# Performance work log

Hardware: AMD Instinct MI355X
Metric: run time of the kernel (lower is better)

The kernel has to match this reference:

```python
import jax, jax.numpy as jnp
import numpy as np

B, T, H, W, C = 2, 8, 64, 64, 192
WIN = (4, 8, 8)
SHIFT = (2, 4, 4)
HEADS = 6
HID = 4 * C
N = WIN[0] * WIN[1] * WIN[2]  # 256 tokens per window
CPB_HID = 512


def window_partition(x, win):
    b, t, h, w, c = x.shape
    x = x.reshape(b, t // win[0], win[0], h // win[1], win[1], w // win[2], win[2], c)
    x = x.transpose(0, 1, 3, 5, 2, 4, 6, 7)
    return x.reshape(-1, win[0] * win[1] * win[2], c)


def window_reverse(wins, win, b, t, h, w):
    x = wins.reshape(b, t // win[0], h // win[1], w // win[2], win[0], win[1], win[2], -1)
    x = x.transpose(0, 1, 4, 2, 5, 3, 6, 7)
    return x.reshape(b, t, h, w, -1)


def _rel_coords_table():
    axes = [np.arange(-(WIN[i] - 1), WIN[i], dtype=np.float32) for i in range(3)]
    tbl = np.stack(np.meshgrid(*axes, indexing='ij'), axis=-1)  # (2wt-1,2wh-1,2ww-1,3)
    for i in range(3):
        tbl[..., i] /= WIN[i] - 1
    tbl *= 8.0
    tbl = np.sign(tbl) * np.log2(np.abs(tbl) + 1.0) / np.log2(8.0)
    return tbl.reshape(-1, 3)


def _rel_pos_index():
    coords = np.stack(np.meshgrid(np.arange(WIN[0]), np.arange(WIN[1]), np.arange(WIN[2]), indexing='ij'))
    cf = coords.reshape(3, -1)
    rel = (cf[:, :, None] - cf[:, None, :]).transpose(1, 2, 0)
    rel[..., 0] += WIN[0] - 1
    rel[..., 1] += WIN[1] - 1
    rel[..., 2] += WIN[2] - 1
    rel[..., 0] *= (2 * WIN[1] - 1) * (2 * WIN[2] - 1)
    rel[..., 1] *= 2 * WIN[2] - 1
    return rel.sum(-1)  # (N, N) int


def _attn_mask():
    img = np.zeros((1, T, H, W, 1), dtype=np.float32)
    cnt = 0
    for d in (slice(-WIN[0]), slice(-WIN[0], -SHIFT[0]), slice(-SHIFT[0], None)):
        for h in (slice(-WIN[1]), slice(-WIN[1], -SHIFT[1]), slice(-SHIFT[1], None)):
            for w in (slice(-WIN[2]), slice(-WIN[2], -SHIFT[2]), slice(-SHIFT[2], None)):
                img[:, d, h, w, :] = cnt
                cnt += 1
    mw = window_partition(img, WIN).squeeze(-1)  # (nW, N)
    am = mw[:, None, :] - mw[:, :, None]
    return np.where(am != 0, -100.0, 0.0).astype(np.float32)


REL_TABLE = jnp.asarray(_rel_coords_table())      # (M, 3)
RPI = jnp.asarray(_rel_pos_index().reshape(-1))   # (N*N,)
MASK = jnp.asarray(_attn_mask())                  # (nW, N, N)


def _ln(x, g, b):
    m = x.mean(-1, keepdims=True)
    v = x.var(-1, keepdims=True)
    return (x - m) / jnp.sqrt(v + 1e-5) * g + b


def setup_inputs() -> dict:
    key = jax.random.key(0)
    ks = jax.random.split(key, 16)
    s = lambda fan: 1.0 / np.sqrt(fan)
    return {
        'x': jax.random.normal(ks[0], (B, T, H, W, C), jnp.float32),
        'qkv_w': jax.random.normal(ks[1], (3 * C, C), jnp.float32) * s(C),
        'qkv_b': jnp.zeros((3 * C,), jnp.float32),
        'proj_w': jax.random.normal(ks[2], (C, C), jnp.float32) * s(C),
        'proj_b': jnp.zeros((C,), jnp.float32),
        'cpb_w1': jax.random.normal(ks[3], (CPB_HID, 3), jnp.float32) * s(3),
        'cpb_b1': jnp.zeros((CPB_HID,), jnp.float32),
        'cpb_w2': jax.random.normal(ks[4], (HEADS, CPB_HID), jnp.float32) * s(CPB_HID),
        'logit_scale': jnp.log(10.0 * jnp.ones((HEADS, 1, 1), jnp.float32)),
        'norm1_g': jnp.ones((C,), jnp.float32),
        'norm1_b': jnp.zeros((C,), jnp.float32),
        'norm2_g': jnp.ones((C,), jnp.float32),
        'norm2_b': jnp.zeros((C,), jnp.float32),
        'fc1_w': jax.random.normal(ks[5], (HID, C), jnp.float32) * s(C),
        'fc1_b': jnp.zeros((HID,), jnp.float32),
        'fc2_w': jax.random.normal(ks[6], (C, HID), jnp.float32) * s(HID),
        'fc2_b': jnp.zeros((C,), jnp.float32),
    }


def reference(x, qkv_w, qkv_b, proj_w, proj_b, cpb_w1, cpb_b1, cpb_w2,
              logit_scale, norm1_g, norm1_b, norm2_g, norm2_b,
              fc1_w, fc1_b, fc2_w, fc2_b):
    shortcut = x
    # cyclic shift
    xs = jnp.roll(x, shift=(-SHIFT[0], -SHIFT[1], -SHIFT[2]), axis=(1, 2, 3))
    xw = window_partition(xs, WIN)  # (B*nW, N, C)
    B_ = xw.shape[0]
    d = C // HEADS
    qkv = (xw @ qkv_w.T + qkv_b).reshape(B_, N, 3, HEADS, d).transpose(2, 0, 3, 1, 4)
    q, k, v = qkv[0], qkv[1], qkv[2]  # (B_, h, N, d)
    # cosine attention (F.normalize eps=1e-12)
    qn = q / jnp.maximum(jnp.linalg.norm(q, axis=-1, keepdims=True), 1e-12)
    kn = k / jnp.maximum(jnp.linalg.norm(k, axis=-1, keepdims=True), 1e-12)
    attn = jnp.einsum('bhnd,bhmd->bhnm', qn, kn)
    scale = jnp.exp(jnp.minimum(logit_scale, jnp.log(100.0)))  # clamp at log(1/0.01)
    attn = attn * scale
    # continuous relative position bias
    tbl = jax.nn.relu(REL_TABLE @ cpb_w1.T + cpb_b1) @ cpb_w2.T  # (M, heads)
    bias = tbl[RPI].reshape(N, N, HEADS).transpose(2, 0, 1)      # (h, N, N)
    attn = attn + 16.0 * jax.nn.sigmoid(bias)[None]
    # shift mask
    nW = MASK.shape[0]
    attn = attn.reshape(B_ // nW, nW, HEADS, N, N) + MASK[None, :, None]
    attn = jax.nn.softmax(attn.reshape(B_, HEADS, N, N), axis=-1)
    out = jnp.einsum('bhnm,bhmd->bhnd', attn, v)
    out = out.transpose(0, 2, 1, 3).reshape(B_, N, C)
    out = out @ proj_w.T + proj_b
    xr = window_reverse(out, WIN, B, T, H, W)
    xr = jnp.roll(xr, shift=SHIFT, axis=(1, 2, 3))
    # SwinV2 res-post-norm residual
    x = shortcut + _ln(xr, norm1_g, norm1_b)
    h1 = jax.nn.gelu(x @ fc1_w.T + fc1_b, approximate=False)
    x = x + _ln(h1 @ fc2_w.T + fc2_b, norm2_g, norm2_b)
    return x
```

## Files before the change

kernel.cpp:

```cpp
#include <hip/hip_runtime.h>
#include <math.h>


typedef short short8 __attribute__((ext_vector_type(8)));
typedef short short4v __attribute__((ext_vector_type(4)));
typedef float f32x4 __attribute__((ext_vector_type(4)));

__device__ __forceinline__ short f2bf(float f) {
    union { float f; unsigned u; } v; v.f = f;
    unsigned r = v.u + 0x7FFF + ((v.u >> 16) & 1);
    return (short)(r >> 16);
}

__device__ __forceinline__ float gelu_fast(float x) {
    float s = x * x;
    float t = fmaf(0.044715f, s, 1.0f);
    float y = -1.5957691216057308f * x * t;
    return x / (1.0f + __expf(y));
}

__global__ __launch_bounds__(64) void pack_w_k(const float* __restrict__ w,
                                               short* __restrict__ dst, int K) {
    int lane = threadIdx.x;
    int ktn = K >> 5;
    int nt = blockIdx.x / ktn, kt = blockIdx.x % ktn;
    int r = lane & 15, q = lane >> 4;
    const float* src = w + (size_t)(nt * 16 + r) * K + kt * 32 + q * 8;
    short8 v;
#pragma unroll
    for (int j = 0; j < 8; j++) v[j] = f2bf(src[j]);
    ((short8*)dst)[(size_t)blockIdx.x * 64 + lane] = v;
}

__global__ __launch_bounds__(64) void cpb_table_k(const float* __restrict__ w1,
                                                  const float* __restrict__ b1,
                                                  const float* __restrict__ w2,
                                                  float* __restrict__ tbl6) {
    int m = blockIdx.x;
    int lane = threadIdx.x;
    int it = m / 225;
    int ih = (m / 15) % 15;
    int iw = m % 15;
    float r0 = (float)(it - 3) * (8.0f / 3.0f);
    float r1 = (float)(ih - 7) * (8.0f / 7.0f);
    float r2 = (float)(iw - 7) * (8.0f / 7.0f);
    float c0 = (r0 < 0.f ? -1.f : 1.f) * log2f(fabsf(r0) + 1.0f) * (1.0f / 3.0f);
    float c1 = (r1 < 0.f ? -1.f : 1.f) * log2f(fabsf(r1) + 1.0f) * (1.0f / 3.0f);
    float c2 = (r2 < 0.f ? -1.f : 1.f) * log2f(fabsf(r2) + 1.0f) * (1.0f / 3.0f);
    float hv[8];
#pragma unroll
    for (int j = 0; j < 8; j++) {
        int t = lane * 8 + j;
        hv[j] = fmaxf(0.0f, c0 * w1[3 * t] + c1 * w1[3 * t + 1] + c2 * w1[3 * t + 2] + b1[t]);
    }
#pragma unroll
    for (int head = 0; head < 6; head++) {
        float s = 0.f;
#pragma unroll
        for (int j = 0; j < 8; j++) s += hv[j] * w2[head * 512 + lane * 8 + j];
        s += __shfl_xor(s, 1);
        s += __shfl_xor(s, 2);
        s += __shfl_xor(s, 4);
        s += __shfl_xor(s, 8);
        s += __shfl_xor(s, 16);
        s += __shfl_xor(s, 32);
        if (lane == 0) tbl6[m * 6 + head] = s;
    }
}

__global__ __launch_bounds__(256) void bias_k(const float* __restrict__ tbl6,
                                              float* __restrict__ biasT) {
    int idx = blockIdx.x * 256 + threadIdx.x;
    int h = idx >> 16;
    int rem = idx & 65535;
    int jj = rem >> 8, ii = rem & 255;
    int dt = (ii >> 6) - (jj >> 6) + 3;
    int dh = ((ii >> 3) & 7) - ((jj >> 3) & 7) + 7;
    int dw = (ii & 7) - (jj & 7) + 7;
    int rel = dt * 225 + dh * 15 + dw;
    float v = tbl6[rel * 6 + h];
    biasT[idx] = 16.0f / (1.0f + expf(-v));
}

#define ZSTR 388
__global__ __launch_bounds__(256) void qkv_mfma_k(const float* __restrict__ x,
                                                  const short* __restrict__ wqp,
                                                  const float* __restrict__ qkv_b,
                                                  short* __restrict__ qbf,
                                                  short* __restrict__ kbf,
                                                  short* __restrict__ vtb) {
    __shared__ float Z[32 * ZSTR];
    int tid = threadIdx.x, lane = tid & 63, w = tid >> 6;
    int r = lane & 15, q = lane >> 4;
    int b_ = blockIdx.x >> 3, n0 = (blockIdx.x & 7) << 5;
    int b = b_ >> 7, win = b_ & 127;
    int wt = win >> 6, wh = (win >> 3) & 7, ww = win & 7;

    short8 af[2][6];
#pragma unroll
    for (int m = 0; m < 2; m++) {
        int n = n0 + m * 16 + r;
        int t0 = ((wt * 4 + (n >> 6)) + 2) & 7;
        int h0 = ((wh * 8 + ((n >> 3) & 7)) + 4) & 63;
        int w0 = ((ww * 8 + (n & 7)) + 4) & 63;
        const float* src = x + ((size_t)((b * 8 + t0) * 64 + h0) * 64 + w0) * 192 + q * 8;
#pragma unroll
        for (int kt = 0; kt < 6; kt++) {
            float4 x0 = *(const float4*)(src + kt * 32);
            float4 x1 = *(const float4*)(src + kt * 32 + 4);
            short8 v;
            v[0] = f2bf(x0.x); v[1] = f2bf(x0.y); v[2] = f2bf(x0.z); v[3] = f2bf(x0.w);
            v[4] = f2bf(x1.x); v[5] = f2bf(x1.y); v[6] = f2bf(x1.z); v[7] = f2bf(x1.w);
            af[m][kt] = v;
        }
    }

    for (int ntl = 0; ntl < 9; ntl++) {
        int nt = w * 9 + ntl;
        float bias = qkv_b[nt * 16 + r];
        short8 bfr[6];
#pragma unroll
        for (int kt = 0; kt < 6; kt++)
            bfr[kt] = ((const short8*)wqp)[(size_t)(nt * 6 + kt) * 64 + lane];
        f32x4 a0 = {bias, bias, bias, bias};
        f32x4 a1 = {bias, bias, bias, bias};
#pragma unroll
        for (int kt = 0; kt < 6; kt++) {
            a0 = __builtin_amdgcn_mfma_f32_16x16x32_bf16(af[0][kt], bfr[kt], a0, 0, 0, 0);
            a1 = __builtin_amdgcn_mfma_f32_16x16x32_bf16(af[1][kt], bfr[kt], a1, 0, 0, 0);
        }
        int col = nt * 16 + r;
        if (nt < 24) {
#pragma unroll
            for (int reg = 0; reg < 4; reg++) {
                Z[(q * 4 + reg) * ZSTR + col] = a0[reg];
                Z[(16 + q * 4 + reg) * ZSTR + col] = a1[reg];
            }
        } else {
            int ch = col - 384;
            int hh = ch >> 5, dd = ch & 31;
            short* vb = vtb + ((size_t)(b_ * 6 + hh) * 32 + dd) * 256 + n0;
            short4v p0, p1;
#pragma unroll
            for (int reg = 0; reg < 4; reg++) { p0[reg] = f2bf(a0[reg]); p1[reg] = f2bf(a1[reg]); }
            *(short4v*)(vb + q * 4) = p0;
            *(short4v*)(vb + 16 + q * 4) = p1;
        }
    }
    __syncthreads();
    for (int rw = tid; rw < 384; rw += 256) {
        int token = rw / 12, rr = rw - token * 12;
        int isq = rr < 6 ? 1 : 0;
        int h = isq ? rr : rr - 6;
        const float* rp = &Z[token * ZSTR + rr * 32];
        float ss = 0.f;
#pragma unroll
        for (int d = 0; d < 32; d++) ss += rp[d] * rp[d];
        float inv = 1.0f / fmaxf(sqrtf(ss), 1e-12f);
        short* dst = (isq ? qbf : kbf) + ((size_t)(b_ * 6 + h) * 256 + n0 + token) * 32;
#pragma unroll
        for (int d8 = 0; d8 < 4; d8++) {
            short8 v;
#pragma unroll
            for (int j = 0; j < 8; j++) v[j] = f2bf(rp[d8 * 8 + j] * inv);
            *(short8*)(dst + d8 * 8) = v;
        }
    }
}

#define KSTR 40
#define VSTR 264
#define PSTR 40
__global__ __launch_bounds__(256) void attn_mfma_k(const short* __restrict__ qbf,
                                                   const short* __restrict__ kbf,
                                                   const short* __restrict__ vtb,
                                                   const float* __restrict__ biasT,
                                                   const float* __restrict__ logit_scale,
                                                   float* __restrict__ att) {
    __shared__ short Ks[256 * KSTR];
    __shared__ short Vs[32 * VSTR];
    __shared__ short Ps[4][16 * PSTR];
    int tid = threadIdx.x, lane = tid & 63, w = tid >> 6;
    int r = lane & 15, q = lane >> 4;
    int b_ = blockIdx.x / 6, h = blockIdx.x % 6;
    size_t base = (size_t)(b_ * 6 + h) * 8192;

    const short8* kg = (const short8*)(kbf + base);
    const short8* vg = (const short8*)(vtb + base);
    for (int i = tid; i < 1024; i += 256) {
        short8 kv = kg[i];
        *(short8*)&Ks[(i >> 2) * KSTR + (i & 3) * 8] = kv;
        short8 vv = vg[i];
        *(short8*)&Vs[(i >> 5) * VSTR + (i & 31) * 8] = vv;
    }

    short8 qf[4];
#pragma unroll
    for (int mt = 0; mt < 4; mt++)
        qf[mt] = *(const short8*)(qbf + base + (size_t)(w * 64 + mt * 16 + r) * 32 + q * 8);

    float scale = __expf(fminf(logit_scale[h], 4.6051702f));
    float M = scale + 16.0f;
    int win = b_ & 127;
    int wt4 = (win >> 6) * 4, wh8 = ((win >> 3) & 7) * 8, ww8 = (win & 7) * 8;
    auto region = [&](int n) {
        int ts = wt4 + (n >> 6), hs = wh8 + ((n >> 3) & 7), wsv = ww8 + (n & 7);
        int rt = ts < 4 ? 0 : (ts < 6 ? 1 : 2);
        int rh = hs < 56 ? 0 : (hs < 60 ? 1 : 2);
        int rw = wsv < 56 ? 0 : (wsv < 60 ? 1 : 2);
        return rt * 9 + rh * 3 + rw;
    };
    int rowreg[4][4];
#pragma unroll
    for (int mt = 0; mt < 4; mt++)
#pragma unroll
        for (int reg = 0; reg < 4; reg++)
            rowreg[mt][reg] = region(w * 64 + mt * 16 + q * 4 + reg);

    f32x4 O[4][2];
    float lp[4][4];
#pragma unroll
    for (int mt = 0; mt < 4; mt++) {
        O[mt][0] = (f32x4){0.f, 0.f, 0.f, 0.f};
        O[mt][1] = (f32x4){0.f, 0.f, 0.f, 0.f};
#pragma unroll
        for (int reg = 0; reg < 4; reg++) lp[mt][reg] = 0.f;
    }
    __syncthreads();

    const float* bh = biasT + ((size_t)h << 16);
    for (int s = 0; s < 8; s++) {
        short8 kf0 = *(const short8*)&Ks[(s * 32 + r) * KSTR + q * 8];
        short8 kf1 = *(const short8*)&Ks[(s * 32 + 16 + r) * KSTR + q * 8];
        short8 vf0 = *(const short8*)&Vs[r * VSTR + s * 32 + q * 8];
        short8 vf1 = *(const short8*)&Vs[(16 + r) * VSTR + s * 32 + q * 8];
        int cr0 = region(s * 32 + r);
        int cr1 = region(s * 32 + 16 + r);
#pragma unroll
        for (int mt = 0; mt < 4; mt++) {
            f32x4 s0 = {0.f, 0.f, 0.f, 0.f};
            f32x4 s1 = {0.f, 0.f, 0.f, 0.f};
            s0 = __builtin_amdgcn_mfma_f32_16x16x32_bf16(qf[mt], kf0, s0, 0, 0, 0);
            s1 = __builtin_amdgcn_mfma_f32_16x16x32_bf16(qf[mt], kf1, s1, 0, 0, 0);
            int qcol = w * 64 + mt * 16 + q * 4;
            float4 b0 = *(const float4*)(bh + (size_t)(s * 32 + r) * 256 + qcol);
            float4 b1 = *(const float4*)(bh + (size_t)(s * 32 + 16 + r) * 256 + qcol);
#pragma unroll
            for (int reg = 0; reg < 4; reg++) {
                float bb0 = (reg == 0 ? b0.x : reg == 1 ? b0.y : reg == 2 ? b0.z : b0.w);
                float bb1 = (reg == 0 ? b1.x : reg == 1 ? b1.y : reg == 2 ? b1.z : b1.w);
                float v0 = s0[reg] * scale + bb0 + (cr0 == rowreg[mt][reg] ? 0.f : -100.f) - M;
                float v1 = s1[reg] * scale + bb1 + (cr1 == rowreg[mt][reg] ? 0.f : -100.f) - M;
                float p0 = __expf(v0);
                float p1 = __expf(v1);
                lp[mt][reg] += p0 + p1;
                Ps[w][(q * 4 + reg) * PSTR + r] = f2bf(p0);
                Ps[w][(q * 4 + reg) * PSTR + 16 + r] = f2bf(p1);
            }
            short8 pa = *(const short8*)&Ps[w][r * PSTR + q * 8];
            O[mt][0] = __builtin_amdgcn_mfma_f32_16x16x32_bf16(pa, vf0, O[mt][0], 0, 0, 0);
            O[mt][1] = __builtin_amdgcn_mfma_f32_16x16x32_bf16(pa, vf1, O[mt][1], 0, 0, 0);
        }
    }

#pragma unroll
    for (int mt = 0; mt < 4; mt++)
#pragma unroll
        for (int reg = 0; reg < 4; reg++) {
            float v = lp[mt][reg];
            v += __shfl_xor(v, 1);
            v += __shfl_xor(v, 2);
            v += __shfl_xor(v, 4);
            v += __shfl_xor(v, 8);
            lp[mt][reg] = 1.0f / v;
        }
#pragma unroll
    for (int mt = 0; mt < 4; mt++)
#pragma unroll
        for (int nt = 0; nt < 2; nt++)
#pragma unroll
            for (int reg = 0; reg < 4; reg++) {
                int query = w * 64 + mt * 16 + q * 4 + reg;
                att[((size_t)b_ * 256 + query) * 192 + h * 32 + nt * 16 + r] =
                    O[mt][nt][reg] * lp[mt][reg];
            }
}

__global__ __launch_bounds__(256) void proj_mfma_k(const float* __restrict__ att,
                                                   const short* __restrict__ wpp,
                                                   const float* __restrict__ proj_b,
                                                   const float* __restrict__ x,
                                                   const float* __restrict__ g1,
                                                   const float* __restrict__ b1n,
                                                   float* __restrict__ out,
                                                   short* __restrict__ xmb) {
    __shared__ float Z[32 * 196];
    __shared__ float ps[32][8];
    __shared__ float pss[32][8];
    __shared__ float mean_s[32], inv_s[32];
    int tid = threadIdx.x, lane = tid & 63, w = tid >> 6;
    int r = lane & 15, q = lane >> 4;
    int b_ = blockIdx.x >> 3, n0 = (blockIdx.x & 7) << 5;

    short8 af[2][6];
#pragma unroll
    for (int m = 0; m < 2; m++) {
        const float* src = att + ((size_t)b_ * 256 + n0 + m * 16 + r) * 192 + q * 8;
#pragma unroll
        for (int kt = 0; kt < 6; kt++) {
            float4 x0 = *(const float4*)(src + kt * 32);
            float4 x1 = *(const float4*)(src + kt * 32 + 4);
            short8 v;
            v[0] = f2bf(x0.x); v[1] = f2bf(x0.y); v[2] = f2bf(x0.z); v[3] = f2bf(x0.w);
            v[4] = f2bf(x1.x); v[5] = f2bf(x1.y); v[6] = f2bf(x1.z); v[7] = f2bf(x1.w);
            af[m][kt] = v;
        }
    }
    for (int ntl = 0; ntl < 3; ntl++) {
        int nt = w * 3 + ntl;
        f32x4 binit = *(const f32x4*)(proj_b + nt * 16 + q * 4);
        short8 bfr[6];
#pragma unroll
        for (int kt = 0; kt < 6; kt++)
            bfr[kt] = ((const short8*)wpp)[(size_t)(nt * 6 + kt) * 64 + lane];
        f32x4 a0 = binit, a1 = binit;
#pragma unroll
        for (int kt = 0; kt < 6; kt++) {
            a0 = __builtin_amdgcn_mfma_f32_16x16x32_bf16(bfr[kt], af[0][kt], a0, 0, 0, 0);
            a1 = __builtin_amdgcn_mfma_f32_16x16x32_bf16(bfr[kt], af[1][kt], a1, 0, 0, 0);
        }
        *(f32x4*)&Z[(r) * 196 + nt * 16 + q * 4] = a0;
        *(f32x4*)&Z[(16 + r) * 196 + nt * 16 + q * 4] = a1;
    }
    __syncthreads();
    {
        int token = tid >> 3, part = tid & 7;
        float s = 0.f, ss = 0.f;
        const float* zr = &Z[token * 196 + part * 24];
#pragma unroll
        for (int c = 0; c < 24; c++) { float v = zr[c]; s += v; ss += v * v; }
        ps[token][part] = s; pss[token][part] = ss;
    }
    __syncthreads();
    if (tid < 32) {
        float s = 0.f, ss = 0.f;
#pragma unroll
        for (int p = 0; p < 8; p++) { s += ps[tid][p]; ss += pss[tid][p]; }
        float mean = s * (1.0f / 192.0f);
        float var = ss * (1.0f / 192.0f) - mean * mean;
        mean_s[tid] = mean;
        inv_s[tid] = 1.0f / sqrtf(var + 1e-5f);
    }
    __syncthreads();
    int b = b_ >> 7, win = b_ & 127;
    int wt = win >> 6, wh = (win >> 3) & 7, ww = win & 7;
    for (int idx = tid; idx < 6144; idx += 256) {
        int token = idx / 192;
        int ch = idx - token * 192;
        int n = n0 + token;
        int t0 = ((wt * 4 + (n >> 6)) + 2) & 7;
        int h0 = ((wh * 8 + ((n >> 3) & 7)) + 4) & 63;
        int w0 = ((ww * 8 + (n & 7)) + 4) & 63;
        size_t gb = ((size_t)((b * 8 + t0) * 64 + h0) * 64 + w0) * 192;
        float v = (Z[token * 196 + ch] - mean_s[token]) * inv_s[token] * g1[ch] + b1n[ch];
        float o = x[gb + ch] + v;
        out[gb + ch] = o;
        xmb[gb + ch] = f2bf(o);
    }
}

#define XSTR 200
#define H2STR 264
#define ZFSTR 196
__global__ __launch_bounds__(512, 4) void mlp_mfma_k(const short* __restrict__ xmb,
                                                     const short* __restrict__ w1p,
                                                     const short* __restrict__ w2p,
                                                     const float* __restrict__ fc1_b,
                                                     const float* __restrict__ fc2_b,
                                                     const float* __restrict__ g2,
                                                     const float* __restrict__ b2,
                                                     float* __restrict__ out) {
    __shared__ short Buf[64 * XSTR + 64 * H2STR];
    short* Xs = Buf;
    short* Hs = Buf + 64 * XSTR;
    float* Z = (float*)Buf;
    __shared__ float mean_s[64], inv_s[64];
    int tid = threadIdx.x;
    int lane = tid & 63, w = tid >> 6;
    int r = lane & 15, q = lane >> 4;
    size_t tok0 = (size_t)blockIdx.x * 64;

    for (int i = tid; i < 1536; i += 512) {
        int token = i / 24, ch8 = (i - token * 24) * 8;
        short8 v = *(const short8*)(xmb + (tok0 + token) * 192 + ch8);
        *(short8*)&Xs[token * XSTR + ch8] = v;
    }
    __syncthreads();

    int mg = w >> 2;
    int ng = w & 3;
    f32x4 acc2[6];
#pragma unroll
    for (int i = 0; i < 6; i++) acc2[i] = (f32x4){0.f, 0.f, 0.f, 0.f};

    for (int c = 0; c < 3; c++) {
        {
            int ntg0 = c * 16 + 2 * w;
            f32x4 a[2][4];
#pragma unroll
            for (int ntl = 0; ntl < 2; ntl++) {
                f32x4 binit = *(const f32x4*)(fc1_b + (ntg0 + ntl) * 16 + q * 4);
#pragma unroll
                for (int m = 0; m < 4; m++) a[ntl][m] = binit;
            }
#pragma unroll
            for (int kt = 0; kt < 6; kt++) {
                short8 w0 = ((const short8*)w1p)[(size_t)((ntg0) * 6 + kt) * 64 + lane];
                short8 w1f = ((const short8*)w1p)[(size_t)((ntg0 + 1) * 6 + kt) * 64 + lane];
                short8 xb[4];
#pragma unroll
                for (int m = 0; m < 4; m++)
                    xb[m] = *(const short8*)&Xs[(m * 16 + r) * XSTR + kt * 32 + q * 8];
#pragma unroll
                for (int m = 0; m < 4; m++) {
                    a[0][m] = __builtin_amdgcn_mfma_f32_16x16x32_bf16(w0, xb[m], a[0][m], 0, 0, 0);
                    a[1][m] = __builtin_amdgcn_mfma_f32_16x16x32_bf16(w1f, xb[m], a[1][m], 0, 0, 0);
                }
            }
#pragma unroll
            for (int ntl = 0; ntl < 2; ntl++) {
                int hcol = (2 * w + ntl) * 16 + q * 4;
#pragma unroll
                for (int m = 0; m < 4; m++) {
                    short4v p;
#pragma unroll
                    for (int reg = 0; reg < 4; reg++) p[reg] = f2bf(gelu_fast(a[ntl][m][reg]));
                    *(short4v*)&Hs[(m * 16 + r) * H2STR + hcol] = p;
                }
            }
        }
        __syncthreads();

#pragma unroll
        for (int kk = 0; kk < 8; kk++) {
            short8 hb0 = *(const short8*)&Hs[((mg * 2) * 16 + r) * H2STR + kk * 32 + q * 8];
            short8 hb1 = *(const short8*)&Hs[((mg * 2 + 1) * 16 + r) * H2STR + kk * 32 + q * 8];
            int kkg = c * 8 + kk;
#pragma unroll
            for (int n = 0; n < 3; n++) {
                int ntz = ng * 3 + n;
                short8 wf = ((const short8*)w2p)[(size_t)(ntz * 24 + kkg) * 64 + lane];
                acc2[n * 2 + 0] = __builtin_amdgcn_mfma_f32_16x16x32_bf16(wf, hb0, acc2[n * 2 + 0], 0, 0, 0);
                acc2[n * 2 + 1] = __builtin_amdgcn_mfma_f32_16x16x32_bf16(wf, hb1, acc2[n * 2 + 1], 0, 0, 0);
            }
        }
        __syncthreads();
    }

#pragma unroll
    for (int n = 0; n < 3; n++) {
        int ntz = ng * 3 + n;
        f32x4 b4 = *(const f32x4*)(fc2_b + ntz * 16 + q * 4);
#pragma unroll
        for (int mh = 0; mh < 2; mh++) {
            int token = (mg * 2 + mh) * 16 + r;
            f32x4 zv = acc2[n * 2 + mh] + b4;
            *(f32x4*)&Z[token * ZFSTR + ntz * 16 + q * 4] = zv;
        }
    }
    __syncthreads();

    {
        int token = w * 8 + (lane >> 3), part = lane & 7;
        float s = 0.f, ss = 0.f;
        const float* zr = &Z[token * ZFSTR + part * 24];
#pragma unroll
        for (int ccc = 0; ccc < 24; ccc++) { float v = zr[ccc]; s += v; ss += v * v; }
        s += __shfl_xor(s, 1); ss += __shfl_xor(ss, 1);
        s += __shfl_xor(s, 2); ss += __shfl_xor(ss, 2);
        s += __shfl_xor(s, 4); ss += __shfl_xor(ss, 4);
        if (part == 0) {
            float mean = s * (1.0f / 192.0f);
            float var = ss * (1.0f / 192.0f) - mean * mean;
            mean_s[token] = mean;
            inv_s[token] = 1.0f / sqrtf(var + 1e-5f);
        }
    }
    __syncthreads();
    for (int rep = 0; rep < 24; rep++) {
        int idx = rep * 512 + tid;
        int token = idx / 192;
        int ch = idx - token * 192;
        float v = (Z[token * ZFSTR + ch] - mean_s[token]) * inv_s[token] * g2[ch] + b2[ch];
        size_t gi = (tok0 + token) * 192 + ch;
        out[gi] = out[gi] + v;
    }
}

extern "C" void kernel_launch(void* const* d_in, const int* in_sizes, int n_in,
                              void* d_out, int out_size, void* d_ws, size_t ws_size,
                              hipStream_t stream) {
    const float* x           = (const float*)d_in[0];
    const float* qkv_w       = (const float*)d_in[1];
    const float* qkv_b       = (const float*)d_in[2];
    const float* proj_w      = (const float*)d_in[3];
    const float* proj_b      = (const float*)d_in[4];
    const float* cpb_w1      = (const float*)d_in[5];
    const float* cpb_b1      = (const float*)d_in[6];
    const float* cpb_w2      = (const float*)d_in[7];
    const float* logit_scale = (const float*)d_in[8];
    const float* norm1_g     = (const float*)d_in[9];
    const float* norm1_b     = (const float*)d_in[10];
    const float* norm2_g     = (const float*)d_in[11];
    const float* norm2_b     = (const float*)d_in[12];
    const float* fc1_w       = (const float*)d_in[13];
    const float* fc1_b       = (const float*)d_in[14];
    const float* fc2_w       = (const float*)d_in[15];
    const float* fc2_b       = (const float*)d_in[16];
    float* out = (float*)d_out;

    float* ws = (float*)d_ws;
    const size_t QKVE = (size_t)256 * 6 * 256 * 32;
    float* att    = ws;
    float* biasT  = att + QKVE;
    float* tbl6   = biasT + (size_t)6 * 256 * 256;
    short* w1pack = (short*)(tbl6 + 9472);
    short* w2pack = w1pack + (size_t)768 * 192;
    short* wqpack = w2pack + (size_t)192 * 768;
    short* wppack = wqpack + (size_t)576 * 192;
    short* qbf    = wppack + (size_t)192 * 192;
    short* kbf    = qbf + QKVE;
    short* vtb    = kbf + QKVE;
    short* xmb    = vtb + QKVE;

    hipLaunchKernelGGL(pack_w_k, dim3(288), dim3(64), 0, stream, fc1_w, w1pack, 192);
    hipLaunchKernelGGL(pack_w_k, dim3(288), dim3(64), 0, stream, fc2_w, w2pack, 768);
    hipLaunchKernelGGL(pack_w_k, dim3(216), dim3(64), 0, stream, qkv_w, wqpack, 192);
    hipLaunchKernelGGL(pack_w_k, dim3(72), dim3(64), 0, stream, proj_w, wppack, 192);
    hipLaunchKernelGGL(cpb_table_k, dim3(1575), dim3(64), 0, stream, cpb_w1, cpb_b1, cpb_w2, tbl6);
    hipLaunchKernelGGL(bias_k, dim3(1536), dim3(256), 0, stream, tbl6, biasT);
    hipLaunchKernelGGL(qkv_mfma_k, dim3(2048), dim3(256), 0, stream, x, wqpack, qkv_b, qbf, kbf, vtb);
    hipLaunchKernelGGL(attn_mfma_k, dim3(1536), dim3(256), 0, stream, qbf, kbf, vtb, biasT, logit_scale, att);
    hipLaunchKernelGGL(proj_mfma_k, dim3(2048), dim3(256), 0, stream, att, wppack, proj_b, x, norm1_g, norm1_b, out, xmb);
    hipLaunchKernelGGL(mlp_mfma_k, dim3(1024), dim3(512), 0, stream, xmb, w1pack, w2pack,
                       fc1_b, fc2_b, norm2_g, norm2_b, out);
}
```

Measured before the change: 418.2 us.

## Shrink MLP hidden chunk and compute LayerNorm stats from registers

The MLP kernel now processes the hidden dimension in six chunks of 128 instead of three of 256. This halves the Hs shared buffer and the fc1 accumulator registers and raises the occupancy hint from 4 to 6 blocks. The final LayerNorm no longer spills fc2 results to a shared Z buffer. It reduces per-token sums from MFMA accumulators via shuffles and a small partial-sum array, then writes the residual output directly from registers with vectorized loads and stores. The cost is more loop iterations and barriers, and smaller per-wave MFMA batches in fc1.

```diff
diff --git a/kernel.cpp b/kernel.cpp
--- a/kernel.cpp
+++ b/kernel.cpp
@@ -370,9 +370,8 @@
 }
 
 #define XSTR 200
-#define H2STR 264
-#define ZFSTR 196
-__global__ __launch_bounds__(512, 4) void mlp_mfma_k(const short* __restrict__ xmb,
+#define H2STR 136
+__global__ __launch_bounds__(512, 6) void mlp_mfma_k(const short* __restrict__ xmb,
                                                      const short* __restrict__ w1p,
                                                      const short* __restrict__ w2p,
                                                      const float* __restrict__ fc1_b,
@@ -380,10 +379,9 @@
                                                      const float* __restrict__ g2,
                                                      const float* __restrict__ b2,
                                                      float* __restrict__ out) {
-    __shared__ short Buf[64 * XSTR + 64 * H2STR];
-    short* Xs = Buf;
-    short* Hs = Buf + 64 * XSTR;
-    float* Z = (float*)Buf;
+    __shared__ short Xs[64 * XSTR];
+    __shared__ short Hs[64 * H2STR];
+    __shared__ float ps[64][4], pss[64][4];
     __shared__ float mean_s[64], inv_s[64];
     int tid = threadIdx.x;
     int lane = tid & 63, w = tid >> 6;
@@ -403,49 +401,40 @@
 #pragma unroll
     for (int i = 0; i < 6; i++) acc2[i] = (f32x4){0.f, 0.f, 0.f, 0.f};
 
-    for (int c = 0; c < 3; c++) {
+    for (int c = 0; c < 6; c++) {
         {
-            int ntg0 = c * 16 + 2 * w;
-            f32x4 a[2][4];
-#pragma unroll
-            for (int ntl = 0; ntl < 2; ntl++) {
-                f32x4 binit = *(const f32x4*)(fc1_b + (ntg0 + ntl) * 16 + q * 4);
-#pragma unroll
-                for (int m = 0; m < 4; m++) a[ntl][m] = binit;
-            }
+            int ntg = c * 8 + w;
+            f32x4 binit = *(const f32x4*)(fc1_b + ntg * 16 + q * 4);
+            f32x4 a[4];
+#pragma unroll
+            for (int m = 0; m < 4; m++) a[m] = binit;
 #pragma unroll
             for (int kt = 0; kt < 6; kt++) {
-                short8 w0 = ((const short8*)w1p)[(size_t)((ntg0) * 6 + kt) * 64 + lane];
-                short8 w1f = ((const short8*)w1p)[(size_t)((ntg0 + 1) * 6 + kt) * 64 + lane];
+                short8 w0 = ((const short8*)w1p)[(size_t)(ntg * 6 + kt) * 64 + lane];
                 short8 xb[4];
 #pragma unroll
                 for (int m = 0; m < 4; m++)
                     xb[m] = *(const short8*)&Xs[(m * 16 + r) * XSTR + kt * 32 + q * 8];
 #pragma unroll
-                for (int m = 0; m < 4; m++) {
-                    a[0][m] = __builtin_amdgcn_mfma_f32_16x16x32_bf16(w0, xb[m], a[0][m], 0, 0, 0);
-                    a[1][m] = __builtin_amdgcn_mfma_f32_16x16x32_bf16(w1f, xb[m], a[1][m], 0, 0, 0);
-                }
+                for (int m = 0; m < 4; m++)
+                    a[m] = __builtin_amdgcn_mfma_f32_16x16x32_bf16(w0, xb[m], a[m], 0, 0, 0);
             }
-#pragma unroll
-            for (int ntl = 0; ntl < 2; ntl++) {
-                int hcol = (2 * w + ntl) * 16 + q * 4;
-#pragma unroll
-                for (int m = 0; m < 4; m++) {
-                    short4v p;
-#pragma unroll
-                    for (int reg = 0; reg < 4; reg++) p[reg] = f2bf(gelu_fast(a[ntl][m][reg]));
-                    *(short4v*)&Hs[(m * 16 + r) * H2STR + hcol] = p;
-                }
+            int hcol = w * 16 + q * 4;
+#pragma unroll
+            for (int m = 0; m < 4; m++) {
+                short4v p;
+#pragma unroll
+                for (int reg = 0; reg < 4; reg++) p[reg] = f2bf(gelu_fast(a[m][reg]));
+                *(short4v*)&Hs[(m * 16 + r) * H2STR + hcol] = p;
             }
         }
         __syncthreads();
 
 #pragma unroll
-        for (int kk = 0; kk < 8; kk++) {
+        for (int kk = 0; kk < 4; kk++) {
             short8 hb0 = *(const short8*)&Hs[((mg * 2) * 16 + r) * H2STR + kk * 32 + q * 8];
             short8 hb1 = *(const short8*)&Hs[((mg * 2 + 1) * 16 + r) * H2STR + kk * 32 + q * 8];
-            int kkg = c * 8 + kk;
+            int kkg = c * 4 + kk;
 #pragma unroll
             for (int n = 0; n < 3; n++) {
                 int ntz = ng * 3 + n;
@@ -457,43 +446,57 @@
         __syncthreads();
     }
 
+    float s0 = 0.f, ss0 = 0.f, s1 = 0.f, ss1 = 0.f;
+#pragma unroll
+    for (int n = 0; n < 3; n++) {
+        f32x4 b4 = *(const f32x4*)(fc2_b + (ng * 3 + n) * 16 + q * 4);
+        f32x4 z0 = acc2[n * 2 + 0] + b4;
+        f32x4 z1 = acc2[n * 2 + 1] + b4;
+        acc2[n * 2 + 0] = z0;
+        acc2[n * 2 + 1] = z1;
+#pragma unroll
+        for (int reg = 0; reg < 4; reg++) {
+            s0 += z0[reg]; ss0 += z0[reg] * z0[reg];
+            s1 += z1[reg]; ss1 += z1[reg] * z1[reg];
+        }
+    }
+    s0 += __shfl_xor(s0, 16); ss0 += __shfl_xor(ss0, 16);
+    s0 += __shfl_xor(s0, 32); ss0 += __shfl_xor(ss0, 32);
+    s1 += __shfl_xor(s1, 16); ss1 += __shfl_xor(ss1, 16);
+    s1 += __shfl_xor(s1, 32); ss1 += __shfl_xor(ss1, 32);
+    if (q == 0) {
+        int t0 = mg * 32 + r;
+        ps[t0][ng] = s0;  pss[t0][ng] = ss0;
+        ps[t0 + 16][ng] = s1;  pss[t0 + 16][ng] = ss1;
+    }
+    __syncthreads();
+    if (tid < 64) {
+        float sm = ps[tid][0] + ps[tid][1] + ps[tid][2] + ps[tid][3];
+        float sq = pss[tid][0] + pss[tid][1] + pss[tid][2] + pss[tid][3];
+        float mean = sm * (1.0f / 192.0f);
+        float var = sq * (1.0f / 192.0f) - mean * mean;
+        mean_s[tid] = mean;
+        inv_s[tid] = 1.0f / sqrtf(var + 1e-5f);
+    }
+    __syncthreads();
 #pragma unroll
     for (int n = 0; n < 3; n++) {
         int ntz = ng * 3 + n;
-        f32x4 b4 = *(const f32x4*)(fc2_b + ntz * 16 + q * 4);
+        f32x4 g4 = *(const f32x4*)(g2 + ntz * 16 + q * 4);
+        f32x4 bb4 = *(const f32x4*)(b2 + ntz * 16 + q * 4);
 #pragma unroll
         for (int mh = 0; mh < 2; mh++) {
-            int token = (mg * 2 + mh) * 16 + r;
-            f32x4 zv = acc2[n * 2 + mh] + b4;
-            *(f32x4*)&Z[token * ZFSTR + ntz * 16 + q * 4] = zv;
-        }
-    }
-    __syncthreads();
-
-    {
-        int token = w * 8 + (lane >> 3), part = lane & 7;
-        float s = 0.f, ss = 0.f;
-        const float* zr = &Z[token * ZFSTR + part * 24];
-#pragma unroll
-        for (int ccc = 0; ccc < 24; ccc++) { float v = zr[ccc]; s += v; ss += v * v; }
-        s += __shfl_xor(s, 1); ss += __shfl_xor(ss, 1);
-        s += __shfl_xor(s, 2); ss += __shfl_xor(ss, 2);
-        s += __shfl_xor(s, 4); ss += __shfl_xor(ss, 4);
-        if (part == 0) {
-            float mean = s * (1.0f / 192.0f);
-            float var = ss * (1.0f / 192.0f) - mean * mean;
-            mean_s[token] = mean;
-            inv_s[token] = 1.0f / sqrtf(var + 1e-5f);
-        }
-    }
-    __syncthreads();
-    for (int rep = 0; rep < 24; rep++) {
-        int idx = rep * 512 + tid;
-        int token = idx / 192;
-        int ch = idx - token * 192;
-        float v = (Z[token * ZFSTR + ch] - mean_s[token]) * inv_s[token] * g2[ch] + b2[ch];
-        size_t gi = (tok0 + token) * 192 + ch;
-        out[gi] = out[gi] + v;
+            int token = mg * 32 + mh * 16 + r;
+            float mean = mean_s[token], inv = inv_s[token];
+            size_t gi = (tok0 + token) * 192 + ntz * 16 + q * 4;
+            f32x4 o = *(const f32x4*)(out + gi);
+            f32x4 z = acc2[n * 2 + mh];
+            f32x4 res;
+#pragma unroll
+            for (int reg = 0; reg < 4; reg++)
+                res[reg] = o[reg] + (z[reg] - mean) * inv * g4[reg] + bb4[reg];
+            *(f32x4*)(out + gi) = res;
+        }
     }
 }
 
```

New measurement: 419.4 us. No clear change (+0.3%).
